# Kernel tuning notes

Measured on AMD Instinct MI355X. Metric: run time of the kernel, lower is better.

The kernel has to match this reference:

```python
import jax, jax.numpy as jnp
import numpy as np

N, C, HW, HEADS = 2048, 16, 8, 4
F = C * HW * HW  # 1024
E = 16384
EPS = 1e-5
NEG_SLOPE = 0.2


def _bn(x, g, b):
    # training-mode BatchNorm2d over (N, H, W)
    m = x.mean(axis=(0, 2, 3), keepdims=True)
    v = x.var(axis=(0, 2, 3), keepdims=True)
    return (x - m) * jax.lax.rsqrt(v + EPS) * g[None, :, None, None] + b[None, :, None, None]


def _conv1x1(x, w, b):
    # 1x1 conv == per-pixel linear: w is [out_c, in_c]
    return jnp.einsum('nchw,oc->nohw', x, w) + b[None, :, None, None]


def _gatv2(xf, edge_index, wl, bl, wr, br, att, bias_gat):
    # xf: [N, F] node features
    xl = (xf @ wl + bl).reshape(N, HEADS, F)  # source-side transform (lin_l)
    xr = (xf @ wr + br).reshape(N, HEADS, F)  # target-side transform (lin_r)
    src, dst = edge_index[0], edge_index[1]
    loops = jnp.arange(N)
    # PyG default: remove existing self loops (mask them) then add self loops
    src_f = jnp.concatenate([src, loops])
    dst_f = jnp.concatenate([dst, loops])
    valid = jnp.concatenate([src != dst, jnp.ones((N,), bool)])
    xj = xl[src_f]                                   # [E+N, HEADS, F] gather
    e = jax.nn.leaky_relu(xj + xr[dst_f], negative_slope=NEG_SLOPE)
    logits = jnp.einsum('ehf,hf->eh', e, att)        # [E+N, HEADS]
    logits = jnp.where(valid[:, None], logits, -jnp.inf)
    mx = jax.lax.stop_gradient(jax.ops.segment_max(logits, dst_f, num_segments=N))
    expv = jnp.where(valid[:, None], jnp.exp(logits - mx[dst_f]), 0.0)
    denom = jax.ops.segment_sum(expv, dst_f, num_segments=N)
    alpha = expv / denom[dst_f]                      # segment softmax over incoming edges
    out = jax.ops.segment_sum(alpha[:, :, None] * xj, dst_f, num_segments=N)  # [N, HEADS, F]
    return out.reshape(N, HEADS * F) + bias_gat


def setup_inputs() -> dict:
    key = jax.random.key(0)
    ks = jax.random.split(key, 8)
    s = 0.02
    return {
        'x': jax.random.normal(ks[0], (N, C, HW, HW), jnp.float32),
        'edge_index': jax.random.randint(ks[1], (2, E), 0, N),
        'w1': jax.random.normal(ks[2], (C, C), jnp.float32) * s,
        'b1': jnp.zeros((C,), jnp.float32),
        'g1': jnp.ones((C,), jnp.float32),
        'be1': jnp.zeros((C,), jnp.float32),
        'wl': jax.random.normal(ks[3], (F, HEADS * F), jnp.float32) * s,
        'bl': jnp.zeros((HEADS * F,), jnp.float32),
        'wr': jax.random.normal(ks[4], (F, HEADS * F), jnp.float32) * s,
        'br': jnp.zeros((HEADS * F,), jnp.float32),
        'att': jax.random.normal(ks[5], (HEADS, F), jnp.float32) * s,
        'bias_gat': jnp.zeros((HEADS * F,), jnp.float32),
        'w2': jax.random.normal(ks[6], (C, HEADS * C), jnp.float32) * s,
        'b2': jnp.zeros((C,), jnp.float32),
        'g2': jnp.ones((C,), jnp.float32),
        'be2': jnp.zeros((C,), jnp.float32),
    }


def reference(x, edge_index, w1, b1, g1, be1, wl, bl, wr, br, att, bias_gat, w2, b2, g2, be2):
    res = x
    y = _bn(_conv1x1(x, w1, b1), g1, be1)            # fc1: Conv2d 1x1 + BN
    yf = y.reshape(N, F)
    g = _gatv2(yf, edge_index, wl, bl, wr, br, att, bias_gat)
    g = g.reshape(N, HEADS * C, HW, HW)
    out = _bn(_conv1x1(g, w2, b2), g2, be2)          # fc2: Conv2d 1x1 + BN
    return out + res                                  # DropPath(0.0) == Identity
```

## Files before the change

### kernel.cpp

```cpp
#include <hip/hip_runtime.h>
#include <stdint.h>

#define N_NODES 2048
#define F_DIM   1024
#define HEADS   4
#define NF      4096
#define ROW     8192
#define E_EDGES 16384
#define MAXE    (E_EDGES + N_NODES)
#define BN_EPS  1e-5f
#define NSLOPE  0.2f

typedef unsigned short ushort_t;
typedef __attribute__((ext_vector_type(8))) short bf16x8;
typedef __attribute__((ext_vector_type(4))) float f32x4;
typedef __attribute__((ext_vector_type(8))) unsigned short us8;

__device__ __forceinline__ float b2f(unsigned short u) {
    union { unsigned int i; float f; } x; x.i = ((unsigned int)u) << 16; return x.f;
}
__device__ __forceinline__ unsigned short f2b(float f) {
    union { float f; unsigned int i; } x; x.f = f;
    unsigned int r = x.i + 0x7fffu + ((x.i >> 16) & 1u);
    return (unsigned short)(r >> 16);
}
__device__ __forceinline__ ushort_t ld_canon(const void* src, size_t i, int f32) {
    return f32 ? f2b(((const float*)src)[i]) : ((const ushort_t*)src)[i];
}
__device__ __forceinline__ float ld_f(const void* src, size_t i, int f32) {
    return f32 ? ((const float*)src)[i] : b2f(((const ushort_t*)src)[i]);
}

__device__ __forceinline__ int sniff_f32_blk(const ushort_t* xu, int* lds_flag) {
    int t = threadIdx.x;
    if (t < 64) {
        unsigned e = (xu[2 * t] >> 7) & 0xFF;
        unsigned long long m = __ballot(e >= 0x90u);
        if (t == 0) *lds_flag = (__popcll(m) >= 3) ? 1 : 0;
    }
    __syncthreads();
    return *lds_flag;
}
__device__ __forceinline__ int sniff_i64_blk(const int* ei_raw, int* lds_flag) {
    int t = threadIdx.x;
    if (t < 64) {
        unsigned long long m = __ballot(ei_raw[2 * t + 1] != 0);
        if (t == 0) *lds_flag = (m == 0ull) ? 1 : 0;
    }
    __syncthreads();
    return *lds_flag;
}

__global__ __launch_bounds__(256) void k_prep(
    const void* __restrict__ wl, const void* __restrict__ wr,
    const int* __restrict__ ei_raw, const ushort_t* __restrict__ xu,
    const void* __restrict__ x, const void* __restrict__ w1, const void* __restrict__ b1,
    ushort_t* __restrict__ wT, int* __restrict__ counts,
    ushort_t* __restrict__ y0b, float* __restrict__ ps, float* __restrict__ pq)
{
    __shared__ ushort_t tl[64][72];
    __shared__ float xs[1024];
    __shared__ float sw[256];
    __shared__ float sb[16];
    __shared__ int sfl;
    int b = blockIdx.x, t = threadIdx.x;
    if (b < 2048) {
        int f32 = sniff_f32_blk(xu, &sfl);
        int z = b >> 10, rem = b & 1023;
        int bx = (rem & 63) * 64, by = (rem >> 6) * 64;
        const void* in = z ? wr : wl;
        ushort_t* outT = wT + (size_t)z * 4194304ull;
        #pragma unroll
        for (int i = 0; i < 2; ++i) {
            int idx = t + i * 256;
            int r = idx >> 3, c8 = (idx & 7) * 8;
            size_t gi = (size_t)(by + r) * 4096 + bx + c8;
            us8 v;
            if (f32) {
                const float* fp = (const float*)in + gi;
                float4 a = *(const float4*)fp;
                float4 bb = *(const float4*)(fp + 4);
                v[0] = f2b(a.x); v[1] = f2b(a.y); v[2] = f2b(a.z); v[3] = f2b(a.w);
                v[4] = f2b(bb.x); v[5] = f2b(bb.y); v[6] = f2b(bb.z); v[7] = f2b(bb.w);
            } else {
                v = *(const us8*)((const ushort_t*)in + gi);
            }
            *(us8*)(&tl[r][c8]) = v;
        }
        __syncthreads();
        #pragma unroll
        for (int i = 0; i < 2; ++i) {
            int idx = t + i * 256;
            int rr = idx >> 3, cc8 = (idx & 7) * 8;
            us8 v;
            #pragma unroll
            for (int j = 0; j < 8; ++j) v[j] = tl[cc8 + j][rr];
            *(us8*)(outT + (size_t)(bx + rr) * 1024 + by + cc8) = v;
        }
    } else if (b < 2120) {
        int i64 = sniff_i64_blk(ei_raw, &sfl);
        int idx = (b - 2048) * 256 + t;
        if (idx < E_EDGES) {
            int s = i64 ? ei_raw[2 * idx] : ei_raw[idx];
            int d = i64 ? ei_raw[2 * (E_EDGES + idx)] : ei_raw[E_EDGES + idx];
            if (s != d) atomicAdd(&counts[d], 1);
        } else if (idx < MAXE) {
            atomicAdd(&counts[idx - E_EDGES], 1);
        }
    } else {
        int bid = b - 2120;
        int f32 = sniff_f32_blk(xu, &sfl);
        sw[t] = ld_f(w1, t, f32);
        if (t < 16) sb[t] = ld_f(b1, t, f32);
        int wave = t >> 6, lane = t & 63;
        float s[4] = {0,0,0,0}, q[4] = {0,0,0,0};
        for (int nn = 0; nn < 8; ++nn) {
            int n = bid * 8 + nn;
            __syncthreads();
            #pragma unroll
            for (int i = 0; i < 4; ++i) {
                int idx = t + i * 256;
                xs[idx] = ld_f(x, (size_t)n * 1024 + idx, f32);
            }
            __syncthreads();
            #pragma unroll
            for (int i = 0; i < 4; ++i) {
                int o = wave * 4 + i;
                float acc = sb[o];
                #pragma unroll
                for (int c = 0; c < 16; ++c) acc += xs[c * 64 + lane] * sw[o * 16 + c];
                y0b[(size_t)n * 1024 + o * 64 + lane] = f2b(acc);
                s[i] += acc; q[i] += acc * acc;
            }
        }
        #pragma unroll
        for (int i = 0; i < 4; ++i)
            for (int mm = 1; mm < 64; mm <<= 1) {
                s[i] += __shfl_xor(s[i], mm);
                q[i] += __shfl_xor(q[i], mm);
            }
        if (lane == 0)
            #pragma unroll
            for (int i = 0; i < 4; ++i) {
                ps[bid * 16 + wave * 4 + i] = s[i];
                pq[bid * 16 + wave * 4 + i] = q[i];
            }
    }
}

__global__ __launch_bounds__(256) void k_scatnorm(
    const int* __restrict__ ei_raw, const int* __restrict__ counts,
    int* __restrict__ cursor, int* __restrict__ offs, int* __restrict__ esrc,
    const ushort_t* __restrict__ y0b,
    const float* __restrict__ ps, const float* __restrict__ pq,
    const void* __restrict__ g1, const void* __restrict__ be1,
    const ushort_t* __restrict__ xu, ushort_t* __restrict__ xf)
{
    __shared__ int offl[2048];
    __shared__ int ts[256];
    __shared__ int sfl;
    __shared__ float red[2][64];
    __shared__ float scs[16], shs[16];
    int t = threadIdx.x;
    if (blockIdx.x < 72) {
        int i64 = sniff_i64_blk(ei_raw, &sfl);
        int loc[8]; int tot = 0;
        #pragma unroll
        for (int j = 0; j < 8; ++j) { loc[j] = counts[t * 8 + j]; tot += loc[j]; }
        ts[t] = tot; __syncthreads();
        for (int s = 1; s < 256; s <<= 1) {
            int v = (t >= s) ? ts[t - s] : 0;
            __syncthreads();
            ts[t] += v;
            __syncthreads();
        }
        int run = ts[t] - tot;
        #pragma unroll
        for (int j = 0; j < 8; ++j) { offl[t * 8 + j] = run; run += loc[j]; }
        __syncthreads();
        if (blockIdx.x == 0) {
            #pragma unroll
            for (int j = 0; j < 8; ++j) offs[t * 8 + j] = offl[t * 8 + j];
            if (t == 255) offs[2048] = run;
        }
        int idx = blockIdx.x * 256 + t;
        if (idx < E_EDGES) {
            int s = i64 ? ei_raw[2 * idx] : ei_raw[idx];
            int d = i64 ? ei_raw[2 * (E_EDGES + idx)] : ei_raw[E_EDGES + idx];
            if (s != d) esrc[offl[d] + atomicAdd(&cursor[d], 1)] = s;
        } else if (idx < MAXE) {
            int n = idx - E_EDGES;
            esrc[offl[n] + atomicAdd(&cursor[n], 1)] = n;
        }
    } else {
        int f32 = sniff_f32_blk(xu, &sfl);
        int lane = t & 63, wv = t >> 6;
        float s = 0.f, q = 0.f;
        #pragma unroll
        for (int i = 0; i < 16; ++i) { s += ps[i * 256 + t]; q += pq[i * 256 + t]; }
        s += __shfl_xor(s, 16); q += __shfl_xor(q, 16);
        s += __shfl_xor(s, 32); q += __shfl_xor(q, 32);
        if (lane < 16) { red[0][wv * 16 + lane] = s; red[1][wv * 16 + lane] = q; }
        __syncthreads();
        if (t < 16) {
            float S = red[0][t] + red[0][16 + t] + red[0][32 + t] + red[0][48 + t];
            float Q = red[1][t] + red[1][16 + t] + red[1][32 + t] + red[1][48 + t];
            const float inv = 1.0f / 131072.0f;
            float mean = S * inv;
            float var  = Q * inv - mean * mean;
            float sc = ld_f(g1, t, f32) * rsqrtf(var + BN_EPS);
            scs[t] = sc;
            shs[t] = ld_f(be1, t, f32) - mean * sc;
        }
        __syncthreads();
        size_t base = (size_t)(blockIdx.x - 72) * 4096 + t * 16;
        int ch = ((int)(base >> 6)) & 15;
        float sc = scs[ch], sh = shs[ch];
        us8 v0 = *(const us8*)(y0b + base), v1 = *(const us8*)(y0b + base + 8);
        us8 o0, o1;
        #pragma unroll
        for (int j = 0; j < 8; ++j) {
            o0[j] = f2b(b2f(v0[j]) * sc + sh);
            o1[j] = f2b(b2f(v1[j]) * sc + sh);
        }
        *(us8*)(xf + base) = o0;
        *(us8*)(xf + base + 8) = o1;
    }
}

__global__ __launch_bounds__(256) void k_gemm(
    const ushort_t* __restrict__ A, const ushort_t* __restrict__ BT,
    const void* __restrict__ blr, const void* __restrict__ brr,
    const ushort_t* __restrict__ xu, ushort_t* __restrict__ out)
{
    __shared__ __align__(16) ushort_t smem[16384];
    ushort_t* As0 = smem;
    ushort_t* As1 = smem + 4096;
    ushort_t* Bs0 = smem + 8192;
    ushort_t* Bs1 = smem + 12288;
    ushort_t* cs  = smem;
    __shared__ int sfl;
    int f32 = sniff_f32_blk(xu, &sfl);
    int tid = threadIdx.x;
    int wv = tid >> 6, ln = tid & 63;
    int fid = blockIdx.y * 64 + blockIdx.x;
    int xcd = fid & 7, idx = fid >> 3;
    int m0 = (((xcd & 1) * 8) + (idx & 7)) * 128;
    int n0 = (((xcd >> 1) * 16) + (idx >> 3)) * 128;
    int wm = (wv >> 1) * 64, wn = (wv & 1) * 64;
    int lr = ln & 15, quad = ln >> 4;
    int swz8 = (quad ^ ((lr >> 1) & 3)) * 8;

    f32x4 acc[4][4];
    #pragma unroll
    for (int i = 0; i < 4; ++i)
        #pragma unroll
        for (int j2 = 0; j2 < 4; ++j2) acc[i][j2] = (f32x4){0.f, 0.f, 0.f, 0.f};

    for (int k0 = 0; k0 < 1024; k0 += 64) {
        #pragma unroll
        for (int i = 0; i < 2; ++i) {
            int cbase = i * 256 + wv * 64;
            int ci = cbase + ln;
            int m = ci >> 2, kc = ci & 3;
            int kq = kc ^ ((m >> 1) & 3);
            const ushort_t* ga = A + (size_t)(m0 + m) * 1024 + k0 + kq * 8;
            __builtin_amdgcn_global_load_lds(
                (const __attribute__((address_space(1))) void*)ga,
                (__attribute__((address_space(3))) void*)(&As0[cbase * 8]), 16, 0, 0);
            __builtin_amdgcn_global_load_lds(
                (const __attribute__((address_space(1))) void*)(ga + 32),
                (__attribute__((address_space(3))) void*)(&As1[cbase * 8]), 16, 0, 0);
            const ushort_t* gb = BT + (size_t)(n0 + m) * 1024 + k0 + kq * 8;
            __builtin_amdgcn_global_load_lds(
                (const __attribute__((address_space(1))) void*)gb,
                (__attribute__((address_space(3))) void*)(&Bs0[cbase * 8]), 16, 0, 0);
            __builtin_amdgcn_global_load_lds(
                (const __attribute__((address_space(1))) void*)(gb + 32),
                (__attribute__((address_space(3))) void*)(&Bs1[cbase * 8]), 16, 0, 0);
        }
        __syncthreads();
        #pragma unroll
        for (int p = 0; p < 2; ++p) {
            const ushort_t* Ap = p ? As1 : As0;
            const ushort_t* Bp = p ? Bs1 : Bs0;
            bf16x8 af[4], bfr[4];
            #pragma unroll
            for (int i = 0; i < 4; ++i)
                af[i] = *(const bf16x8*)(&Ap[(wm + i * 16 + lr) * 32 + swz8]);
            #pragma unroll
            for (int j2 = 0; j2 < 4; ++j2)
                bfr[j2] = *(const bf16x8*)(&Bp[(wn + j2 * 16 + lr) * 32 + swz8]);
            #pragma unroll
            for (int i = 0; i < 4; ++i)
                #pragma unroll
                for (int j2 = 0; j2 < 4; ++j2)
                    acc[i][j2] = __builtin_amdgcn_mfma_f32_16x16x32_bf16(af[i], bfr[j2], acc[i][j2], 0, 0, 0);
        }
        __syncthreads();
    }
    float bj[4];
    #pragma unroll
    for (int j2 = 0; j2 < 4; ++j2) {
        int colg = n0 + wn + j2 * 16 + lr;
        bj[j2] = (colg < 4096) ? ld_f(blr, colg, f32) : ld_f(brr, colg - 4096, f32);
    }
    #pragma unroll
    for (int ph = 0; ph < 2; ++ph) {
        if ((wv >> 1) == ph) {
            #pragma unroll
            for (int i = 0; i < 4; ++i)
                #pragma unroll
                for (int j2 = 0; j2 < 4; ++j2) {
                    int col = wn + j2 * 16 + lr;
                    #pragma unroll
                    for (int r = 0; r < 4; ++r)
                        cs[(i * 16 + quad * 4 + r) * 136 + col] = f2b(acc[i][j2][r] + bj[j2]);
                }
        }
        __syncthreads();
        #pragma unroll
        for (int rr = 0; rr < 4; ++rr) {
            int slot = rr * 256 + tid;
            int row = slot >> 4, seg = slot & 15;
            us8 v = *(const us8*)&cs[row * 136 + seg * 8];
            *(us8*)(out + (size_t)(m0 + ph * 64 + row) * ROW + n0 + seg * 8) = v;
        }
        __syncthreads();
    }
}

__global__ __launch_bounds__(256) void k_gat(
    const ushort_t* __restrict__ xlr,
    const void* __restrict__ att, const void* __restrict__ bg,
    const ushort_t* __restrict__ xu,
    const int* __restrict__ offsets, const int* __restrict__ esrc,
    ushort_t* __restrict__ g)
{
    int d = blockIdx.x;
    int t = threadIdx.x;
    int h = t >> 6, l = t & 63;
    int f32;
    {
        unsigned e = (xu[2 * l] >> 7) & 0xFF;
        unsigned long long m = __ballot(e >= 0x90u);
        f32 = (__popcll(m) >= 3) ? 1 : 0;
    }
    int off = offsets[d], deg = offsets[d + 1] - off;
    size_t hF = (size_t)h * F_DIM + l * 16;

    float xrv[16], attv[16];
    {
        const ushort_t* xp = xlr + ((size_t)d * ROW + NF + hF);
        us8 x0 = *(const us8*)xp, x1 = *(const us8*)(xp + 8);
        #pragma unroll
        for (int j = 0; j < 8; ++j) {
            xrv[j] = b2f(x0[j]); xrv[8 + j] = b2f(x1[j]);
            attv[j]     = ld_f(att, hF + j, f32);
            attv[8 + j] = ld_f(att, hF + 8 + j, f32);
        }
    }
    float acc[16];
    #pragma unroll
    for (int j = 0; j < 16; ++j) acc[j] = 0.f;
    float s_run = 0.f;

    for (int c0 = 0; c0 < deg; c0 += 64) {
        int cnt = min(64, deg - c0);
        int eidx = esrc[off + c0 + (l < cnt ? l : 0)];
        int e = 0;
        for (; e + 3 < cnt; e += 4) {
            int i0 = __shfl(eidx, e),     i1 = __shfl(eidx, e + 1);
            int i2 = __shfl(eidx, e + 2), i3 = __shfl(eidx, e + 3);
            const ushort_t* p0 = xlr + ((size_t)i0 * ROW + hF);
            const ushort_t* p1 = xlr + ((size_t)i1 * ROW + hF);
            const ushort_t* p2 = xlr + ((size_t)i2 * ROW + hF);
            const ushort_t* p3 = xlr + ((size_t)i3 * ROW + hF);
            us8 v0[4], v1[4];
            v0[0] = *(const us8*)p0; v1[0] = *(const us8*)(p0 + 8);
            v0[1] = *(const us8*)p1; v1[1] = *(const us8*)(p1 + 8);
            v0[2] = *(const us8*)p2; v1[2] = *(const us8*)(p2 + 8);
            v0[3] = *(const us8*)p3; v1[3] = *(const us8*)(p3 + 8);
            float tt[4];
            #pragma unroll
            for (int k = 0; k < 4; ++k) {
                float t0 = 0.f;
                #pragma unroll
                for (int j = 0; j < 8; ++j) {
                    float u;
                    u = b2f(v0[k][j]) + xrv[j];     u = u > 0.f ? u : NSLOPE * u; t0 += u * attv[j];
                    u = b2f(v1[k][j]) + xrv[8 + j]; u = u > 0.f ? u : NSLOPE * u; t0 += u * attv[8 + j];
                }
                tt[k] = t0;
            }
            #pragma unroll
            for (int mm = 1; mm < 64; mm <<= 1) {
                tt[0] += __shfl_xor(tt[0], mm);
                tt[1] += __shfl_xor(tt[1], mm);
                tt[2] += __shfl_xor(tt[2], mm);
                tt[3] += __shfl_xor(tt[3], mm);
            }
            float w0 = __expf(tt[0]), w1 = __expf(tt[1]);
            float w2v = __expf(tt[2]), w3 = __expf(tt[3]);
            s_run += w0 + w1 + w2v + w3;
            #pragma unroll
            for (int j = 0; j < 8; ++j) {
                acc[j]     += w0 * b2f(v0[0][j]) + w1 * b2f(v0[1][j])
                            + w2v * b2f(v0[2][j]) + w3 * b2f(v0[3][j]);
                acc[8 + j] += w0 * b2f(v1[0][j]) + w1 * b2f(v1[1][j])
                            + w2v * b2f(v1[2][j]) + w3 * b2f(v1[3][j]);
            }
        }
        for (; e < cnt; ++e) {
            int i0 = __shfl(eidx, e);
            const ushort_t* p = xlr + ((size_t)i0 * ROW + hF);
            us8 a0 = *(const us8*)p, a1 = *(const us8*)(p + 8);
            float t0 = 0.f;
            #pragma unroll
            for (int j = 0; j < 8; ++j) {
                float u;
                u = b2f(a0[j]) + xrv[j];     u = u > 0.f ? u : NSLOPE * u; t0 += u * attv[j];
                u = b2f(a1[j]) + xrv[8 + j]; u = u > 0.f ? u : NSLOPE * u; t0 += u * attv[8 + j];
            }
            #pragma unroll
            for (int mm = 1; mm < 64; mm <<= 1) t0 += __shfl_xor(t0, mm);
            float w0 = __expf(t0);
            s_run += w0;
            #pragma unroll
            for (int j = 0; j < 8; ++j) {
                acc[j]     += w0 * b2f(a0[j]);
                acc[8 + j] += w0 * b2f(a1[j]);
            }
        }
    }
    float inv = 1.0f / s_run;
    ushort_t* gp = g + ((size_t)d * NF + hF);
    us8 outv0, outv1;
    #pragma unroll
    for (int j = 0; j < 8; ++j) {
        outv0[j] = f2b(acc[j] * inv + ld_f(bg, hF + j, f32));
        outv1[j] = f2b(acc[8 + j] * inv + ld_f(bg, hF + 8 + j, f32));
    }
    *(us8*)gp = outv0;
    *(us8*)(gp + 8) = outv1;
}

__global__ __launch_bounds__(256) void k_fc2(
    const ushort_t* __restrict__ g, const void* __restrict__ w2, const void* __restrict__ b2,
    const ushort_t* __restrict__ xu,
    ushort_t* __restrict__ zb, float* __restrict__ ps, float* __restrict__ pq)
{
    __shared__ float gs[4096];
    __shared__ float sw[1024];
    __shared__ float sb[16];
    __shared__ int sfl;
    int f32 = sniff_f32_blk(xu, &sfl);
    int tid = threadIdx.x;
    #pragma unroll
    for (int i = 0; i < 4; ++i) sw[tid + i * 256] = ld_f(w2, tid + i * 256, f32);
    if (tid < 16) sb[tid] = ld_f(b2, tid, f32);
    int wave = tid >> 6, lane = tid & 63;
    float s[4] = {0,0,0,0}, q[4] = {0,0,0,0};
    for (int nn = 0; nn < 2; ++nn) {
        int n = blockIdx.x * 2 + nn;
        __syncthreads();
        {
            const ushort_t* gp = g + (size_t)n * 4096 + tid * 16;
            us8 v0 = *(const us8*)gp, v1 = *(const us8*)(gp + 8);
            #pragma unroll
            for (int j = 0; j < 8; ++j) {
                gs[tid * 16 + j] = b2f(v0[j]);
                gs[tid * 16 + 8 + j] = b2f(v1[j]);
            }
        }
        __syncthreads();
        float acc[4];
        #pragma unroll
        for (int i = 0; i < 4; ++i) acc[i] = sb[wave * 4 + i];
        #pragma unroll 8
        for (int k = 0; k < 64; ++k) {
            float gv = gs[k * 64 + lane];
            #pragma unroll
            for (int i = 0; i < 4; ++i)
                acc[i] += gv * sw[(wave * 4 + i) * 64 + k];
        }
        #pragma unroll
        for (int i = 0; i < 4; ++i) {
            zb[(size_t)n * 1024 + (wave * 4 + i) * 64 + lane] = f2b(acc[i]);
            s[i] += acc[i]; q[i] += acc[i] * acc[i];
        }
    }
    #pragma unroll
    for (int i = 0; i < 4; ++i)
        for (int mm = 1; mm < 64; mm <<= 1) {
            s[i] += __shfl_xor(s[i], mm);
            q[i] += __shfl_xor(q[i], mm);
        }
    if (lane == 0)
        #pragma unroll
        for (int i = 0; i < 4; ++i) {
            ps[blockIdx.x * 16 + wave * 4 + i] = s[i];
            pq[blockIdx.x * 16 + wave * 4 + i] = q[i];
        }
}

__global__ __launch_bounds__(256) void k_out(
    const ushort_t* __restrict__ zb, const void* __restrict__ x,
    const float* __restrict__ ps, const float* __restrict__ pq,
    const void* __restrict__ g2, const void* __restrict__ be2,
    void* __restrict__ out)
{
    __shared__ float red[2][64];
    __shared__ float scs[16], shs[16];
    __shared__ int sfl;
    int f32 = sniff_f32_blk((const ushort_t*)x, &sfl);
    int t = threadIdx.x, lane = t & 63, wv = t >> 6;
    float s = 0.f, q = 0.f;
    #pragma unroll
    for (int i = 0; i < 64; ++i) { s += ps[i * 256 + t]; q += pq[i * 256 + t]; }
    s += __shfl_xor(s, 16); q += __shfl_xor(q, 16);
    s += __shfl_xor(s, 32); q += __shfl_xor(q, 32);
    if (lane < 16) { red[0][wv * 16 + lane] = s; red[1][wv * 16 + lane] = q; }
    __syncthreads();
    if (t < 16) {
        float S = red[0][t] + red[0][16 + t] + red[0][32 + t] + red[0][48 + t];
        float Q = red[1][t] + red[1][16 + t] + red[1][32 + t] + red[1][48 + t];
        const float inv = 1.0f / 131072.0f;
        float mean = S * inv;
        float var  = Q * inv - mean * mean;
        float sc = ld_f(g2, t, f32) * rsqrtf(var + BN_EPS);
        scs[t] = sc;
        shs[t] = ld_f(be2, t, f32) - mean * sc;
    }
    __syncthreads();
    size_t base = (size_t)blockIdx.x * 4096;
    #pragma unroll
    for (int i = 0; i < 16; ++i) {
        size_t k = base + t + i * 256;
        int ch = ((int)k >> 6) & 15;
        float val = b2f(zb[k]) * scs[ch] + shs[ch] + ld_f(x, k, f32);
        if (f32) ((float*)out)[k] = val;
        else     ((ushort_t*)out)[k] = f2b(val);
    }
}

extern "C" void kernel_launch(void* const* d_in, const int* in_sizes, int n_in,
                              void* d_out, int out_size, void* d_ws, size_t ws_size,
                              hipStream_t stream)
{
    const void* x   = d_in[0];
    const void* ei  = d_in[1];
    const void* w1  = d_in[2];
    const void* b1  = d_in[3];
    const void* g1  = d_in[4];
    const void* be1 = d_in[5];
    const void* wl  = d_in[6];
    const void* bl  = d_in[7];
    const void* wr  = d_in[8];
    const void* br  = d_in[9];
    const void* att = d_in[10];
    const void* bg  = d_in[11];
    const void* w2  = d_in[12];
    const void* b2  = d_in[13];
    const void* g2  = d_in[14];
    const void* be2 = d_in[15];
    (void)in_sizes; (void)n_in; (void)out_size; (void)ws_size;

    char* wsb = (char*)d_ws;
    size_t o = 0;
    auto alloc = [&](size_t bytes) -> void* {
        void* p = wsb + o;
        o = (o + bytes + 255) & ~(size_t)255;
        return p;
    };
    ushort_t* y0b   = (ushort_t*)alloc(2097152ull * 2);
    ushort_t* xf    = (ushort_t*)alloc(2097152ull * 2);
    ushort_t* zb    = (ushort_t*)alloc(2097152ull * 2);
    ushort_t* wT    = (ushort_t*)alloc(8388608ull * 2);
    ushort_t* gbuf  = wT;
    ushort_t* xlr   = (ushort_t*)alloc(16777216ull * 2);
    float* p1s = (float*)alloc(256 * 16 * 4);
    float* p1q = (float*)alloc(256 * 16 * 4);
    float* p2s = (float*)alloc(1024 * 16 * 4);
    float* p2q = (float*)alloc(1024 * 16 * 4);
    int* counts = (int*)alloc(2048 * 4);
    int* cursor = (int*)alloc(2048 * 4);
    int* offs   = (int*)alloc(2049 * 4);
    int* esrc   = (int*)alloc(MAXE * 4);

    hipMemsetAsync(counts, 0, 2 * 2048 * 4, stream);
    k_prep<<<2376, 256, 0, stream>>>(wl, wr, (const int*)ei, (const ushort_t*)x,
                                     x, w1, b1, wT, counts, y0b, p1s, p1q);
    k_scatnorm<<<584, 256, 0, stream>>>((const int*)ei, counts, cursor, offs, esrc,
                                        y0b, p1s, p1q, g1, be1, (const ushort_t*)x, xf);
    k_gemm<<<dim3(64, 16), 256, 0, stream>>>(xf, wT, bl, br, (const ushort_t*)x, xlr);
    k_gat<<<N_NODES, 256, 0, stream>>>(xlr, att, bg, (const ushort_t*)x, offs, esrc, gbuf);
    k_fc2<<<1024, 256, 0, stream>>>(gbuf, w2, b2, (const ushort_t*)x, zb, p2s, p2q);
    k_out<<<512, 256, 0, stream>>>(zb, x, p2s, p2q, g2, be2, d_out);
}
```

Measured before the change: 260.5 us.

## Restructure GAT kernel to one wave per head over four nodes, precast att/bias

The GAT aggregation kernel now launches 64-thread blocks, each handling one head for four consecutive destination nodes, instead of one 256-thread block per node covering all heads. Attention and bias vectors are converted to fp32 once by two extra prep blocks, which removes the per-block dtype sniff and converted loads. The aim is to cut per-block overhead and amortize the att/bias loads across nodes. The cost is less parallelism per block and serialized node processing within a wave, which could hurt latency hiding for gathers.

```diff
diff --git a/kernel.cpp b/kernel.cpp
--- a/kernel.cpp
+++ b/kernel.cpp
@@ -55,8 +55,10 @@
     const void* __restrict__ wl, const void* __restrict__ wr,
     const int* __restrict__ ei_raw, const ushort_t* __restrict__ xu,
     const void* __restrict__ x, const void* __restrict__ w1, const void* __restrict__ b1,
+    const void* __restrict__ att, const void* __restrict__ bg,
     ushort_t* __restrict__ wT, int* __restrict__ counts,
-    ushort_t* __restrict__ y0b, float* __restrict__ ps, float* __restrict__ pq)
+    ushort_t* __restrict__ y0b, float* __restrict__ ps, float* __restrict__ pq,
+    float* __restrict__ attf, float* __restrict__ bgf)
 {
     __shared__ ushort_t tl[64][72];
     __shared__ float xs[1024];
@@ -64,7 +66,16 @@
     __shared__ float sb[16];
     __shared__ int sfl;
     int b = blockIdx.x, t = threadIdx.x;
-    if (b < 2048) {
+    if (b >= 2376) {
+        int f32 = sniff_f32_blk(xu, &sfl);
+        const void* src = (b == 2376) ? att : bg;
+        float* dst = (b == 2376) ? attf : bgf;
+        #pragma unroll
+        for (int j = 0; j < 16; ++j) {
+            int idx = t * 16 + j;
+            dst[idx] = ld_f(src, idx, f32);
+        }
+    } else if (b < 2048) {
         int f32 = sniff_f32_blk(xu, &sfl);
         int z = b >> 10, rem = b & 1023;
         int bx = (rem & 63) * 64, by = (rem >> 6) * 64;
@@ -330,119 +341,131 @@
     }
 }
 
-__global__ __launch_bounds__(256) void k_gat(
+__global__ __launch_bounds__(64) void k_gat(
     const ushort_t* __restrict__ xlr,
-    const void* __restrict__ att, const void* __restrict__ bg,
-    const ushort_t* __restrict__ xu,
+    const float* __restrict__ attf, const float* __restrict__ bgf,
     const int* __restrict__ offsets, const int* __restrict__ esrc,
     ushort_t* __restrict__ g)
 {
-    int d = blockIdx.x;
-    int t = threadIdx.x;
-    int h = t >> 6, l = t & 63;
-    int f32;
+    int bx = blockIdx.x;
+    int h = bx & 3;
+    int dbase = (bx >> 2) * 4;
+    int l = threadIdx.x;
+    size_t hF = (size_t)h * F_DIM + l * 16;
+
+    float attv[16], bgv[16];
     {
-        unsigned e = (xu[2 * l] >> 7) & 0xFF;
-        unsigned long long m = __ballot(e >= 0x90u);
-        f32 = (__popcll(m) >= 3) ? 1 : 0;
-    }
-    int off = offsets[d], deg = offsets[d + 1] - off;
-    size_t hF = (size_t)h * F_DIM + l * 16;
-
-    float xrv[16], attv[16];
-    {
-        const ushort_t* xp = xlr + ((size_t)d * ROW + NF + hF);
-        us8 x0 = *(const us8*)xp, x1 = *(const us8*)(xp + 8);
-        #pragma unroll
-        for (int j = 0; j < 8; ++j) {
-            xrv[j] = b2f(x0[j]); xrv[8 + j] = b2f(x1[j]);
-            attv[j]     = ld_f(att, hF + j, f32);
-            attv[8 + j] = ld_f(att, hF + 8 + j, f32);
-        }
-    }
-    float acc[16];
-    #pragma unroll
-    for (int j = 0; j < 16; ++j) acc[j] = 0.f;
-    float s_run = 0.f;
-
-    for (int c0 = 0; c0 < deg; c0 += 64) {
-        int cnt = min(64, deg - c0);
-        int eidx = esrc[off + c0 + (l < cnt ? l : 0)];
-        int e = 0;
-        for (; e + 3 < cnt; e += 4) {
-            int i0 = __shfl(eidx, e),     i1 = __shfl(eidx, e + 1);
-            int i2 = __shfl(eidx, e + 2), i3 = __shfl(eidx, e + 3);
-            const ushort_t* p0 = xlr + ((size_t)i0 * ROW + hF);
-            const ushort_t* p1 = xlr + ((size_t)i1 * ROW + hF);
-            const ushort_t* p2 = xlr + ((size_t)i2 * ROW + hF);
-            const ushort_t* p3 = xlr + ((size_t)i3 * ROW + hF);
-            us8 v0[4], v1[4];
-            v0[0] = *(const us8*)p0; v1[0] = *(const us8*)(p0 + 8);
-            v0[1] = *(const us8*)p1; v1[1] = *(const us8*)(p1 + 8);
-            v0[2] = *(const us8*)p2; v1[2] = *(const us8*)(p2 + 8);
-            v0[3] = *(const us8*)p3; v1[3] = *(const us8*)(p3 + 8);
-            float tt[4];
-            #pragma unroll
-            for (int k = 0; k < 4; ++k) {
+        const float* ap = attf + hF;
+        const float* bp = bgf + hF;
+        float4 a0 = *(const float4*)ap,       a1 = *(const float4*)(ap + 4);
+        float4 a2 = *(const float4*)(ap + 8), a3 = *(const float4*)(ap + 12);
+        float4 b0 = *(const float4*)bp,       b1 = *(const float4*)(bp + 4);
+        float4 b2 = *(const float4*)(bp + 8), b3 = *(const float4*)(bp + 12);
+        attv[0]=a0.x; attv[1]=a0.y; attv[2]=a0.z; attv[3]=a0.w;
+        attv[4]=a1.x; attv[5]=a1.y; attv[6]=a1.z; attv[7]=a1.w;
+        attv[8]=a2.x; attv[9]=a2.y; attv[10]=a2.z; attv[11]=a2.w;
+        attv[12]=a3.x; attv[13]=a3.y; attv[14]=a3.z; attv[15]=a3.w;
+        bgv[0]=b0.x; bgv[1]=b0.y; bgv[2]=b0.z; bgv[3]=b0.w;
+        bgv[4]=b1.x; bgv[5]=b1.y; bgv[6]=b1.z; bgv[7]=b1.w;
+        bgv[8]=b2.x; bgv[9]=b2.y; bgv[10]=b2.z; bgv[11]=b2.w;
+        bgv[12]=b3.x; bgv[13]=b3.y; bgv[14]=b3.z; bgv[15]=b3.w;
+    }
+
+    for (int dd = 0; dd < 4; ++dd) {
+        int d = dbase + dd;
+        int off = offsets[d], deg = offsets[d + 1] - off;
+
+        float xrv[16];
+        {
+            const ushort_t* xp = xlr + ((size_t)d * ROW + NF + hF);
+            us8 x0 = *(const us8*)xp, x1 = *(const us8*)(xp + 8);
+            #pragma unroll
+            for (int j = 0; j < 8; ++j) { xrv[j] = b2f(x0[j]); xrv[8 + j] = b2f(x1[j]); }
+        }
+        float acc[16];
+        #pragma unroll
+        for (int j = 0; j < 16; ++j) acc[j] = 0.f;
+        float s_run = 0.f;
+
+        for (int c0 = 0; c0 < deg; c0 += 64) {
+            int cnt = min(64, deg - c0);
+            int eidx = esrc[off + c0 + (l < cnt ? l : 0)];
+            int e = 0;
+            for (; e + 3 < cnt; e += 4) {
+                int i0 = __shfl(eidx, e),     i1 = __shfl(eidx, e + 1);
+                int i2 = __shfl(eidx, e + 2), i3 = __shfl(eidx, e + 3);
+                const ushort_t* p0 = xlr + ((size_t)i0 * ROW + hF);
+                const ushort_t* p1 = xlr + ((size_t)i1 * ROW + hF);
+                const ushort_t* p2 = xlr + ((size_t)i2 * ROW + hF);
+                const ushort_t* p3 = xlr + ((size_t)i3 * ROW + hF);
+                us8 v0[4], v1[4];
+                v0[0] = *(const us8*)p0; v1[0] = *(const us8*)(p0 + 8);
+                v0[1] = *(const us8*)p1; v1[1] = *(const us8*)(p1 + 8);
+                v0[2] = *(const us8*)p2; v1[2] = *(const us8*)(p2 + 8);
+                v0[3] = *(const us8*)p3; v1[3] = *(const us8*)(p3 + 8);
+                float tt[4];
+                #pragma unroll
+                for (int k = 0; k < 4; ++k) {
+                    float t0 = 0.f;
+                    #pragma unroll
+                    for (int j = 0; j < 8; ++j) {
+                        float u;
+                        u = b2f(v0[k][j]) + xrv[j];     u = u > 0.f ? u : NSLOPE * u; t0 += u * attv[j];
+                        u = b2f(v1[k][j]) + xrv[8 + j]; u = u > 0.f ? u : NSLOPE * u; t0 += u * attv[8 + j];
+                    }
+                    tt[k] = t0;
+                }
+                #pragma unroll
+                for (int mm = 1; mm < 64; mm <<= 1) {
+                    tt[0] += __shfl_xor(tt[0], mm);
+                    tt[1] += __shfl_xor(tt[1], mm);
+                    tt[2] += __shfl_xor(tt[2], mm);
+                    tt[3] += __shfl_xor(tt[3], mm);
+                }
+                float w0 = __expf(tt[0]), w1 = __expf(tt[1]);
+                float w2v = __expf(tt[2]), w3 = __expf(tt[3]);
+                s_run += w0 + w1 + w2v + w3;
+                #pragma unroll
+                for (int j = 0; j < 8; ++j) {
+                    acc[j]     += w0 * b2f(v0[0][j]) + w1 * b2f(v0[1][j])
+                                + w2v * b2f(v0[2][j]) + w3 * b2f(v0[3][j]);
+                    acc[8 + j] += w0 * b2f(v1[0][j]) + w1 * b2f(v1[1][j])
+                                + w2v * b2f(v1[2][j]) + w3 * b2f(v1[3][j]);
+                }
+            }
+            for (; e < cnt; ++e) {
+                int i0 = __shfl(eidx, e);
+                const ushort_t* p = xlr + ((size_t)i0 * ROW + hF);
+                us8 a0 = *(const us8*)p, a1 = *(const us8*)(p + 8);
                 float t0 = 0.f;
                 #pragma unroll
                 for (int j = 0; j < 8; ++j) {
                     float u;
-                    u = b2f(v0[k][j]) + xrv[j];     u = u > 0.f ? u : NSLOPE * u; t0 += u * attv[j];
-                    u = b2f(v1[k][j]) + xrv[8 + j]; u = u > 0.f ? u : NSLOPE * u; t0 += u * attv[8 + j];
+                    u = b2f(a0[j]) + xrv[j];     u = u > 0.f ? u : NSLOPE * u; t0 += u * attv[j];
+                    u = b2f(a1[j]) + xrv[8 + j]; u = u > 0.f ? u : NSLOPE * u; t0 += u * attv[8 + j];
                 }
-                tt[k] = t0;
-            }
-            #pragma unroll
-            for (int mm = 1; mm < 64; mm <<= 1) {
-                tt[0] += __shfl_xor(tt[0], mm);
-                tt[1] += __shfl_xor(tt[1], mm);
-                tt[2] += __shfl_xor(tt[2], mm);
-                tt[3] += __shfl_xor(tt[3], mm);
-            }
-            float w0 = __expf(tt[0]), w1 = __expf(tt[1]);
-            float w2v = __expf(tt[2]), w3 = __expf(tt[3]);
-            s_run += w0 + w1 + w2v + w3;
-            #pragma unroll
-            for (int j = 0; j < 8; ++j) {
-                acc[j]     += w0 * b2f(v0[0][j]) + w1 * b2f(v0[1][j])
-                            + w2v * b2f(v0[2][j]) + w3 * b2f(v0[3][j]);
-                acc[8 + j] += w0 * b2f(v1[0][j]) + w1 * b2f(v1[1][j])
-                            + w2v * b2f(v1[2][j]) + w3 * b2f(v1[3][j]);
-            }
-        }
-        for (; e < cnt; ++e) {
-            int i0 = __shfl(eidx, e);
-            const ushort_t* p = xlr + ((size_t)i0 * ROW + hF);
-            us8 a0 = *(const us8*)p, a1 = *(const us8*)(p + 8);
-            float t0 = 0.f;
-            #pragma unroll
-            for (int j = 0; j < 8; ++j) {
-                float u;
-                u = b2f(a0[j]) + xrv[j];     u = u > 0.f ? u : NSLOPE * u; t0 += u * attv[j];
-                u = b2f(a1[j]) + xrv[8 + j]; u = u > 0.f ? u : NSLOPE * u; t0 += u * attv[8 + j];
-            }
-            #pragma unroll
-            for (int mm = 1; mm < 64; mm <<= 1) t0 += __shfl_xor(t0, mm);
-            float w0 = __expf(t0);
-            s_run += w0;
-            #pragma unroll
-            for (int j = 0; j < 8; ++j) {
-                acc[j]     += w0 * b2f(a0[j]);
-                acc[8 + j] += w0 * b2f(a1[j]);
-            }
-        }
-    }
-    float inv = 1.0f / s_run;
-    ushort_t* gp = g + ((size_t)d * NF + hF);
-    us8 outv0, outv1;
-    #pragma unroll
-    for (int j = 0; j < 8; ++j) {
-        outv0[j] = f2b(acc[j] * inv + ld_f(bg, hF + j, f32));
-        outv1[j] = f2b(acc[8 + j] * inv + ld_f(bg, hF + 8 + j, f32));
-    }
-    *(us8*)gp = outv0;
-    *(us8*)(gp + 8) = outv1;
+                #pragma unroll
+                for (int mm = 1; mm < 64; mm <<= 1) t0 += __shfl_xor(t0, mm);
+                float w0 = __expf(t0);
+                s_run += w0;
+                #pragma unroll
+                for (int j = 0; j < 8; ++j) {
+                    acc[j]     += w0 * b2f(a0[j]);
+                    acc[8 + j] += w0 * b2f(a1[j]);
+                }
+            }
+        }
+        float inv = 1.0f / s_run;
+        ushort_t* gp = g + ((size_t)d * NF + hF);
+        us8 outv0, outv1;
+        #pragma unroll
+        for (int j = 0; j < 8; ++j) {
+            outv0[j] = f2b(acc[j] * inv + bgv[j]);
+            outv1[j] = f2b(acc[8 + j] * inv + bgv[8 + j]);
+        }
+        *(us8*)gp = outv0;
+        *(us8*)(gp + 8) = outv1;
+    }
 }
 
 __global__ __launch_bounds__(256) void k_fc2(
@@ -587,14 +610,16 @@
     int* cursor = (int*)alloc(2048 * 4);
     int* offs   = (int*)alloc(2049 * 4);
     int* esrc   = (int*)alloc(MAXE * 4);
+    float* attf = (float*)alloc(4096 * 4);
+    float* bgf  = (float*)alloc(4096 * 4);
 
     hipMemsetAsync(counts, 0, 2 * 2048 * 4, stream);
-    k_prep<<<2376, 256, 0, stream>>>(wl, wr, (const int*)ei, (const ushort_t*)x,
-                                     x, w1, b1, wT, counts, y0b, p1s, p1q);
+    k_prep<<<2378, 256, 0, stream>>>(wl, wr, (const int*)ei, (const ushort_t*)x,
+                                     x, w1, b1, att, bg, wT, counts, y0b, p1s, p1q, attf, bgf);
     k_scatnorm<<<584, 256, 0, stream>>>((const int*)ei, counts, cursor, offs, esrc,
                                         y0b, p1s, p1q, g1, be1, (const ushort_t*)x, xf);
     k_gemm<<<dim3(64, 16), 256, 0, stream>>>(xf, wT, bl, br, (const ushort_t*)x, xlr);
-    k_gat<<<N_NODES, 256, 0, stream>>>(xlr, att, bg, (const ushort_t*)x, offs, esrc, gbuf);
+    k_gat<<<2048, 64, 0, stream>>>(xlr, attf, bgf, offs, esrc, gbuf);
     k_fc2<<<1024, 256, 0, stream>>>(gbuf, w2, b2, (const ushort_t*)x, zb, p2s, p2q);
     k_out<<<512, 256, 0, stream>>>(zb, x, p2s, p2q, g2, be2, d_out);
 }
```

Measured after the change: 245.4 us (median of 2 runs). 5.8% less time.
